# Optimization experiments

Measured on AMD Instinct MI355X. Metric: run time of the kernel, lower is better.

Reference implementation:

```python
import jax, jax.numpy as jnp
import numpy as np

B, C, H, W = 8, 384, 32, 32
KEYS, HEADS, U = 16, 4, 1
VS = C // HEADS
N = H * W
BN_EPS = 1e-5


def setup_inputs() -> dict:
    key = jax.random.key(0)
    ks = jax.random.split(key, 8)
    x = jax.random.normal(ks[0], (B, C, H, W), dtype=jnp.float32)
    # 1x1 convs (spectral-normalized in torch; SN only rescales the weight,
    # so a plain weight matrix computes the same functional form)
    Wq = jax.random.normal(ks[1], (KEYS * HEADS, C), dtype=jnp.float32) * 0.02
    Wk = jax.random.normal(ks[2], (KEYS * U, C), dtype=jnp.float32) * 0.02
    Wv = jax.random.normal(ks[3], (VS * U, C), dtype=jnp.float32) * 0.02
    # BatchNorm affine params (torch code xavier-inits weight, zeros bias)
    gamma_q = jax.random.normal(ks[4], (KEYS * HEADS,), dtype=jnp.float32)
    beta_q = jnp.zeros((KEYS * HEADS,), dtype=jnp.float32)
    gamma_v = jax.random.normal(ks[5], (VS * U,), dtype=jnp.float32)
    beta_v = jnp.zeros((VS * U,), dtype=jnp.float32)
    pos_emb = jax.random.normal(ks[6], (N, N, KEYS, U), dtype=jnp.float32)
    return {"x": x, "Wq": Wq, "Wk": Wk, "Wv": Wv,
            "gamma_q": gamma_q, "beta_q": beta_q,
            "gamma_v": gamma_v, "beta_v": beta_v,
            "pos_emb": pos_emb}


def _bn(z, gamma, beta):
    # z: (B, Ch, N); BatchNorm2d in training mode: biased batch stats over (B, N)
    mean = jnp.mean(z, axis=(0, 2), keepdims=True)
    var = jnp.var(z, axis=(0, 2), keepdims=True)
    zn = (z - mean) * jax.lax.rsqrt(var + BN_EPS)
    return zn * gamma[None, :, None] + beta[None, :, None]


def reference(x, Wq, Wk, Wv, gamma_q, beta_q, gamma_v, beta_v, pos_emb):
    xf = x.reshape(B, C, N)                       # 1x1 conv == per-pixel matmul
    q = jnp.einsum('oc,bcn->bon', Wq, xf)         # (B, KEYS*HEADS, N)
    k = jnp.einsum('oc,bcn->bon', Wk, xf)         # (B, KEYS*U, N)
    v = jnp.einsum('oc,bcn->bon', Wv, xf)         # (B, VS*U, N)
    q = _bn(q, gamma_q, beta_q)
    v = _bn(v, gamma_v, beta_v)
    q = q.reshape(B, HEADS, KEYS, N)
    k = k.reshape(B, U, KEYS, N)
    v = v.reshape(B, U, VS, N)
    k = jax.nn.softmax(k, axis=-1)
    lambdac = jnp.einsum('bukm,buvm->bkv', k, v)          # content lambda
    Yc = jnp.einsum('bhkn,bkv->bhvn', q, lambdac)
    lambdap = jnp.einsum('nmku,buvm->bnkv', pos_emb, v)   # position lambda (B,N,K,V)
    Yp = jnp.einsum('bhkn,bnkv->bhvn', q, lambdap)
    Y = (Yc + Yp).reshape(B, C, H, W)
    return Y
```

## Files before the change

### kernel.cpp

```cpp
#include <hip/hip_runtime.h>

typedef __attribute__((ext_vector_type(8))) short short8;
typedef __attribute__((ext_vector_type(16))) float floatx16;
typedef __attribute__((ext_vector_type(4))) float floatx4;
typedef unsigned short ushort16_t;
typedef unsigned int uint32;

#define BB 8
#define CC 384
#define NPIX 1024
#define TOTCH 176
#define BN_EPS 1e-5f

__device__ __forceinline__ ushort16_t f2bf(float x) {
    uint32 u = __float_as_uint(x);
    u += 0x7FFFu + ((u >> 16) & 1u);
    return (ushort16_t)(u >> 16);
}
__device__ __forceinline__ uint32 pk2(float a, float b) {
    uint32 ua = __float_as_uint(a); ua += 0x7FFFu + ((ua >> 16) & 1u);
    uint32 ub = __float_as_uint(b); ub += 0x7FFFu + ((ub >> 16) & 1u);
    return (ua >> 16) | (ub & 0xFFFF0000u);
}
__device__ __forceinline__ void dma16(const ushort16_t* g, ushort16_t* l) {
    __builtin_amdgcn_global_load_lds(
        (const __attribute__((address_space(1))) uint32*)g,
        (__attribute__((address_space(3))) uint32*)l, 16, 0, 0);
}


__global__ __launch_bounds__(256) void k_xt(const float* __restrict__ x,
    const float* __restrict__ Wq, const float* __restrict__ Wk,
    const float* __restrict__ Wv,
    ushort16_t* __restrict__ xbf, ushort16_t* __restrict__ wbf)
{
    int bx = blockIdx.x, t = threadIdx.x;
    if (bx < 384) {
        int gi = bx * 256 + t;
        int colg = gi & 2047;
        int cg   = gi >> 11;
        int b  = colg >> 8;
        int n0 = (colg & 255) * 4;
        int c0 = cg * 8;
        int col0 = colg * 4;
        float vv[8][4];
        #pragma unroll
        for (int j = 0; j < 8; ++j) {
            float4 f = *(const float4*)(x + (size_t)b * (CC * NPIX)
                                          + (size_t)(c0 + j) * NPIX + n0);
            vv[j][0] = f.x; vv[j][1] = f.y; vv[j][2] = f.z; vv[j][3] = f.w;
        }
        #pragma unroll
        for (int cc = 0; cc < 4; ++cc) {
            uint4 w;
            w.x = pk2(vv[0][cc], vv[1][cc]);
            w.y = pk2(vv[2][cc], vv[3][cc]);
            w.z = pk2(vv[4][cc], vv[5][cc]);
            w.w = pk2(vv[6][cc], vv[7][cc]);
            *(uint4*)&xbf[(size_t)(col0 + cc) * CC + c0] = w;
        }
    } else {
        int idx8 = (bx - 384) * 256 + t;
        int row = idx8 / 48;
        int j   = idx8 - row * 48;
        float4 f0, f1;
        if (row < 176) {
            const float* src;
            if (row < 64)       src = Wq + (size_t)row * CC;
            else if (row < 80)  src = Wk + (size_t)(row - 64) * CC;
            else                src = Wv + (size_t)(row - 80) * CC;
            f0 = *(const float4*)(src + j * 8);
            f1 = *(const float4*)(src + j * 8 + 4);
        } else {
            f0.x = f0.y = f0.z = f0.w = 0.f;
            f1 = f0;
        }
        uint4 w;
        w.x = pk2(f0.x, f0.y); w.y = pk2(f0.z, f0.w);
        w.z = pk2(f1.x, f1.y); w.w = pk2(f1.z, f1.w);
        *(uint4*)&wbf[(size_t)row * CC + j * 8] = w;
    }
}

__global__ __launch_bounds__(256) void k_proj(const ushort16_t* __restrict__ xbf,
    const ushort16_t* __restrict__ wbf, float* __restrict__ qkv)
{
    int t = threadIdx.x;
    int wave = t >> 6, lane = t & 63;
    int ct = blockIdx.x * 4 + wave;
    int r0 = blockIdx.y * 16;
    int col = ct * 16 + (lane & 15);
    int kh  = lane >> 4;
    const ushort16_t* ap = wbf + (size_t)(r0 + (lane & 15)) * CC + kh * 8;
    const ushort16_t* bp = xbf + (size_t)col * CC + kh * 8;
    floatx4 acc = {0.f, 0.f, 0.f, 0.f};
    short8 a0 = *(const short8*)ap;
    short8 b0 = *(const short8*)bp;
    #pragma unroll
    for (int k = 1; k < 12; ++k) {
        short8 a1 = *(const short8*)(ap + k * 32);
        short8 b1 = *(const short8*)(bp + k * 32);
        acc = __builtin_amdgcn_mfma_f32_16x16x32_bf16(a0, b0, acc, 0, 0, 0);
        a0 = a1; b0 = b1;
    }
    acc = __builtin_amdgcn_mfma_f32_16x16x32_bf16(a0, b0, acc, 0, 0, 0);
    int b = col >> 10, n = col & 1023;
    #pragma unroll
    for (int r = 0; r < 4; ++r) {
        int ch = r0 + (lane >> 4) * 4 + r;
        qkv[((size_t)b * TOTCH + ch) * NPIX + n] = acc[r];
    }
}

__global__ __launch_bounds__(256) void k_bnsm(const float* __restrict__ qkv,
    const float* __restrict__ gq, const float* __restrict__ bq,
    const float* __restrict__ gv, const float* __restrict__ bv,
    float* __restrict__ sA, float* __restrict__ sB, float* __restrict__ ksm)
{
    int bx = blockIdx.x, tid = threadIdx.x;
    int wid = tid >> 6, lane = tid & 63;
    if (bx < 160) {
        int ch = bx;
        int row; float gamma, beta;
        if (ch < 64) { row = ch; gamma = gq[ch]; beta = bq[ch]; }
        else { int j = ch - 64; row = 80 + j; gamma = gv[j]; beta = bv[j]; }
        float s = 0.f, ss = 0.f;
        for (int i = tid; i < BB * NPIX; i += 256) {
            int b = i >> 10, n = i & 1023;
            float val = qkv[((size_t)b * TOTCH + row) * NPIX + n];
            s += val; ss += val * val;
        }
        #pragma unroll
        for (int off = 32; off > 0; off >>= 1) {
            s  += __shfl_down(s, off);
            ss += __shfl_down(ss, off);
        }
        __shared__ float rs[4], rss[4];
        if (lane == 0) { rs[wid] = s; rss[wid] = ss; }
        __syncthreads();
        if (tid == 0) {
            float S  = rs[0] + rs[1] + rs[2] + rs[3];
            float SS = rss[0] + rss[1] + rss[2] + rss[3];
            float inv = 1.f / (BB * NPIX);
            float mean = S * inv;
            float var  = SS * inv - mean * mean;
            float a = gamma * rsqrtf(var + BN_EPS);
            sA[row] = a;
            sB[row] = beta - mean * a;
        }
    } else {
        int idx = bx - 160;
        int kc = idx & 15, b = idx >> 4;
        const float* rowp = qkv + ((size_t)b * TOTCH + 64 + kc) * NPIX;
        float v[4];
        #pragma unroll
        for (int j = 0; j < 4; ++j) v[j] = rowp[tid + 256 * j];
        float mx = fmaxf(fmaxf(v[0], v[1]), fmaxf(v[2], v[3]));
        #pragma unroll
        for (int off = 32; off > 0; off >>= 1) mx = fmaxf(mx, __shfl_down(mx, off));
        __shared__ float sm[4], ssum[4];
        if (lane == 0) sm[wid] = mx;
        __syncthreads();
        mx = fmaxf(fmaxf(sm[0], sm[1]), fmaxf(sm[2], sm[3]));
        float e[4], s = 0.f;
        #pragma unroll
        for (int j = 0; j < 4; ++j) { e[j] = __expf(v[j] - mx); s += e[j]; }
        #pragma unroll
        for (int off = 32; off > 0; off >>= 1) s += __shfl_down(s, off);
        if (lane == 0) ssum[wid] = s;
        __syncthreads();
        float inv = 1.f / (ssum[0] + ssum[1] + ssum[2] + ssum[3]);
        float* op = ksm + ((size_t)b * 16 + kc) * NPIX;
        #pragma unroll
        for (int j = 0; j < 4; ++j) op[tid + 256 * j] = e[j] * inv;
    }
}

__global__ __launch_bounds__(256) void k_pack(const float* __restrict__ qkv,
    const float* __restrict__ sA, const float* __restrict__ sB,
    ushort16_t* __restrict__ qt_g, ushort16_t* __restrict__ vt_g)
{
    int bx = blockIdx.x, t = threadIdx.x;
    if (bx < 128) {
        int bh = t & 31, nn = (t >> 5) & 7;
        int n = bx * 8 + nn;
        int b = bh >> 2, h = bh & 3;
        float vals[16];
        #pragma unroll
        for (int k = 0; k < 16; ++k) {
            int ch = h * 16 + k;
            vals[k] = qkv[((size_t)b * TOTCH + ch) * NPIX + n] * sA[ch] + sB[ch];
        }
        uint4 w0, w1;
        w0.x = pk2(vals[0], vals[1]);  w0.y = pk2(vals[2], vals[3]);
        w0.z = pk2(vals[4], vals[5]);  w0.w = pk2(vals[6], vals[7]);
        w1.x = pk2(vals[8], vals[9]);  w1.y = pk2(vals[10], vals[11]);
        w1.z = pk2(vals[12], vals[13]); w1.w = pk2(vals[14], vals[15]);
        *(uint4*)&qt_g[(size_t)n * 512 + bh * 8]       = w0;
        *(uint4*)&qt_g[(size_t)n * 512 + 256 + bh * 8] = w1;
    } else {
        int gi = (bx - 128) * 256 + t;
        int m8 = gi & 127;
        int vg = (gi >> 7) % 96;
        int b  = gi / (96 * 128);
        int m  = m8 * 8;
        int row = 80 + vg;
        float a = sA[row], bb = sB[row];
        const float* p = qkv + ((size_t)b * TOTCH + row) * NPIX + m;
        float4 f0 = *(const float4*)p;
        float4 f1 = *(const float4*)(p + 4);
        uint4 w;
        w.x = pk2(f0.x * a + bb, f0.y * a + bb);
        w.y = pk2(f0.z * a + bb, f0.w * a + bb);
        w.z = pk2(f1.x * a + bb, f1.y * a + bb);
        w.w = pk2(f1.z * a + bb, f1.w * a + bb);
        int mt = m >> 5, mq = (m >> 3) & 3;
        int vhh = vg / 48, vtt = (vg % 48) >> 4, vl = vg & 15;
        size_t idx = ((((size_t)b * 32 + mt) * 2 + vhh) * 3 + vtt) * 512
                   + mq * 128 + vl * 8;
        *(uint4*)&vt_g[idx] = w;
    }
}

__global__ __launch_bounds__(256) void k_lambdac(const float* __restrict__ ksm,
    const float* __restrict__ qkv, const float* __restrict__ sA,
    const float* __restrict__ sB, ushort16_t* __restrict__ lc_g)
{
    int v = blockIdx.x, b = blockIdx.y, tid = threadIdx.x;
    int row = 80 + v;
    float a = sA[row], bb = sB[row];
    const float* vp = qkv + ((size_t)b * TOTCH + row) * NPIX;
    const float* kp = ksm + (size_t)b * 16 * NPIX;
    float acc[16];
    #pragma unroll
    for (int k = 0; k < 16; ++k) acc[k] = 0.f;
    for (int m = tid; m < NPIX; m += 256) {
        float vv = vp[m] * a + bb;
        #pragma unroll
        for (int k = 0; k < 16; ++k) acc[k] += kp[k * NPIX + m] * vv;
    }
    #pragma unroll
    for (int k = 0; k < 16; ++k) {
        #pragma unroll
        for (int off = 32; off > 0; off >>= 1) acc[k] += __shfl_down(acc[k], off);
    }
    __shared__ float red[16][4];
    int wid = tid >> 6, lane = tid & 63;
    if (lane == 0) {
        #pragma unroll
        for (int k = 0; k < 16; ++k) red[k][wid] = acc[k];
    }
    __syncthreads();
    int vhh = v / 48, vtt = (v % 48) >> 4, vl = v & 15;
    size_t plane = ((size_t)(b * 2 + vhh) * 3 + vtt) * 512;
    if (tid < 16) {
        int k = tid;
        float val = red[k][0] + red[k][1] + red[k][2] + red[k][3];
        lc_g[plane + (k >> 3) * 128 + vl * 8 + (k & 7)] = f2bf(val);
    } else if (tid < 18) {
        int mq = 2 + (tid - 16);
        uint4 z; z.x = z.y = z.z = z.w = 0u;
        *(uint4*)&lc_g[plane + mq * 128 + vl * 8] = z;
    }
}

__global__ __launch_bounds__(512, 2) void k_main(const float* __restrict__ pos,
    const ushort16_t* __restrict__ qt_g, const ushort16_t* __restrict__ vt_g,
    const ushort16_t* __restrict__ lc_g, float* __restrict__ out)
{
    __shared__ __align__(16) ushort16_t q_s[4096];
    __shared__ __align__(16) ushort16_t P_s[4096];
    __shared__ __align__(16) ushort16_t V_s[12288];
    __shared__ __align__(16) ushort16_t S_s[8192];
    int tid  = threadIdx.x;
    int lane = tid & 63;
    int wave = tid >> 6;
    int n0 = blockIdx.x * 8;
    int vh = blockIdx.y;

    dma16(qt_g + (size_t)(n0 + wave) * 512 + lane * 8, &q_s[wave * 512]);

    floatx4 acc[2][3];
    #pragma unroll
    for (int hg = 0; hg < 2; ++hg)
        #pragma unroll
        for (int vt = 0; vt < 3; ++vt)
            acc[hg][vt] = floatx4{0.f, 0.f, 0.f, 0.f};

    int col1 = lane & 31, half = lane >> 5;
    int pb = col1 >> 2, ph = col1 & 3;
    int pplane = pb * 2 + (ph >> 1);
    int pf = pplane & 7;
    int pcb = ph & 1;
    int sm = tid & 31, snn = (tid >> 5) & 7, skh = (tid >> 8) & 1;
    int b2 = wave;

    for (int mt = 0; mt < 32; ++mt) {
        int m0 = mt * 32;
        __syncthreads();
        {
            const ushort16_t* src = vt_g
                + (size_t)(((b2 * 32 + mt) * 2 + vh) * 3) * 512;
            #pragma unroll
            for (int j = 0; j < 3; ++j)
                dma16(src + j * 512 + lane * 8, &V_s[b2 * 1536 + j * 512]);
        }
        {
            const float* p = pos + ((size_t)(n0 + snn) * 1024 + (m0 + sm)) * 16
                           + skh * 8;
            float4 f0 = *(const float4*)p;
            float4 f1 = *(const float4*)(p + 4);
            uint4 w;
            w.x = pk2(f0.x, f0.y); w.y = pk2(f0.z, f0.w);
            w.z = pk2(f1.x, f1.y); w.w = pk2(f1.z, f1.w);
            *(uint4*)&P_s[(snn * 2 + skh) * 256 + sm * 8] = w;
        }
        __syncthreads();
        {
            short8 afr = *(const short8*)&P_s[wave * 512 + half * 256 + col1 * 8];
            short8 bfr = *(const short8*)&q_s[wave * 512 + half * 256 + col1 * 8];
            floatx16 d;
            #pragma unroll
            for (int i = 0; i < 16; ++i) d[i] = 0.f;
            d = __builtin_amdgcn_mfma_f32_32x32x16_bf16(afr, bfr, d, 0, 0, 0);
            int nx = wave ^ pf;
            #pragma unroll
            for (int q = 0; q < 4; ++q) {
                int c = q * 16 + pcb * 8 + nx;
                uint2 wv;
                wv.x = pk2(d[q * 4 + 0], d[q * 4 + 1]);
                wv.y = pk2(d[q * 4 + 2], d[q * 4 + 3]);
                *(uint2*)&S_s[pplane * 512 + c * 8 + half * 4] = wv;
            }
        }
        __syncthreads();
        {
            short8 av[3];
            #pragma unroll
            for (int vt = 0; vt < 3; ++vt)
                av[vt] = *(const short8*)&V_s[b2 * 1536 + vt * 512 + lane * 8];
            #pragma unroll
            for (int hg = 0; hg < 2; ++hg) {
                int p2 = b2 * 2 + hg, f2 = p2 & 7;
                short8 bs = *(const short8*)&S_s[p2 * 512
                    + ((lane >> 4) * 16 + ((lane & 15) ^ f2)) * 8];
                #pragma unroll
                for (int vt = 0; vt < 3; ++vt)
                    acc[hg][vt] = __builtin_amdgcn_mfma_f32_16x16x32_bf16(
                        av[vt], bs, acc[hg][vt], 0, 0, 0);
            }
        }
    }

    __syncthreads();
    {
        const ushort16_t* src = lc_g + (size_t)((b2 * 2 + vh) * 3) * 512;
        #pragma unroll
        for (int j = 0; j < 3; ++j)
            dma16(src + j * 512 + lane * 8, &V_s[b2 * 1536 + j * 512]);
    }
    {
        int bh = tid & 31, nn = (tid >> 5) & 7, kh = (tid >> 8) & 1;
        int b_ = bh >> 2, h_ = bh & 3;
        int pl = b_ * 2 + (h_ >> 1), f = pl & 7;
        short8 qv = *(const short8*)&q_s[nn * 512 + kh * 256 + bh * 8];
        int c = kh * 16 + (h_ & 1) * 8 + (nn ^ f);
        *(short8*)&S_s[pl * 512 + c * 8] = qv;
        int zp = tid >> 5, zr = tid & 31;
        int zc = (2 + (zr >> 4)) * 16 + ((zr & 15) ^ (zp & 7));
        uint4 z; z.x = z.y = z.z = z.w = 0u;
        *(uint4*)&S_s[zp * 512 + zc * 8] = z;
    }
    __syncthreads();
    {
        short8 av[3];
        #pragma unroll
        for (int vt = 0; vt < 3; ++vt)
            av[vt] = *(const short8*)&V_s[b2 * 1536 + vt * 512 + lane * 8];
        #pragma unroll
        for (int hg = 0; hg < 2; ++hg) {
            int p2 = b2 * 2 + hg, f2 = p2 & 7;
            short8 bs = *(const short8*)&S_s[p2 * 512
                + ((lane >> 4) * 16 + ((lane & 15) ^ f2)) * 8];
            #pragma unroll
            for (int vt = 0; vt < 3; ++vt)
                acc[hg][vt] = __builtin_amdgcn_mfma_f32_16x16x32_bf16(
                    av[vt], bs, acc[hg][vt], 0, 0, 0);
        }
    }

    {
        int cn = lane & 15;
        int nloc = cn & 7;
        #pragma unroll
        for (int hg = 0; hg < 2; ++hg) {
            int h = hg * 2 + (cn >> 3);
            #pragma unroll
            for (int vt = 0; vt < 3; ++vt) {
                #pragma unroll
                for (int r = 0; r < 4; ++r) {
                    int v = vh * 48 + vt * 16 + (lane >> 4) * 4 + r;
                    out[(size_t)(b2 * 384 + h * 96 + v) * 1024 + n0 + nloc]
                        = acc[hg][vt][r];
                }
            }
        }
    }
}

extern "C" void kernel_launch(void* const* d_in, const int* in_sizes, int n_in,
                              void* d_out, int out_size, void* d_ws, size_t ws_size,
                              hipStream_t stream) {
    const float* x   = (const float*)d_in[0];
    const float* Wq  = (const float*)d_in[1];
    const float* Wk  = (const float*)d_in[2];
    const float* Wv  = (const float*)d_in[3];
    const float* gq  = (const float*)d_in[4];
    const float* bq  = (const float*)d_in[5];
    const float* gv  = (const float*)d_in[6];
    const float* bv  = (const float*)d_in[7];
    const float* pos = (const float*)d_in[8];
    float* out = (float*)d_out;
    float* ws  = (float*)d_ws;

    float* qkv = ws;
    float* sA  = ws + 1441792;
    float* sB  = ws + 1441968;
    float* ksm = ws + 1442144;
    ushort16_t* qt_g = (ushort16_t*)(ws + 1573216);
    ushort16_t* vt_g = (ushort16_t*)(ws + 1835360);
    ushort16_t* lc_g = (ushort16_t*)(ws + 2228576);
    ushort16_t* xbf  = (ushort16_t*)(ws + 2240864);
    ushort16_t* wbf  = (ushort16_t*)(ws + 3813728);

    k_xt<<<dim3(420), dim3(256), 0, stream>>>(x, Wq, Wk, Wv, xbf, wbf);
    k_proj<<<dim3(128, 11), dim3(256), 0, stream>>>(xbf, wbf, qkv);
    k_bnsm<<<dim3(288), dim3(256), 0, stream>>>(qkv, gq, bq, gv, bv, sA, sB, ksm);
    k_pack<<<dim3(512), dim3(256), 0, stream>>>(qkv, sA, sB, qt_g, vt_g);
    k_lambdac<<<dim3(96, 8), dim3(256), 0, stream>>>(ksm, qkv, sA, sB, lc_g);
    k_main<<<dim3(128, 2), dim3(512), 0, stream>>>(pos, qt_g, vt_g, lc_g, out);
}
```

Before: 203.9 us.

## Double-buffer pos/V tiles in main kernel, merge pack and lambdac, LDS-transpose x

The main kernel now double-buffers the pos_emb tile and the V tile. The next tile's global loads and DMA are issued while MFMA runs on the current one, which removes one barrier per iteration, and q is held in a register instead of LDS. k_pack and k_lambdac are merged into a single launch to save a kernel launch. The x-to-bf16 transpose now goes through an LDS tile so global writes are coalesced, the weight-conversion blocks each handle more work, and the BN/softmax loads use float4 vectors. The costs are more LDS in the main kernel, which may lower occupancy, and extra registers for the prefetched values.

New measurement: 184.8 us. -9.4%, faster.

```diff
diff --git a/kernel.cpp b/kernel.cpp
--- a/kernel.cpp
+++ b/kernel.cpp
@@ -26,6 +26,9 @@
     __builtin_amdgcn_global_load_lds(
         (const __attribute__((address_space(1))) uint32*)g,
         (__attribute__((address_space(3))) uint32*)l, 16, 0, 0);
+}
+__device__ __forceinline__ int div48(int x) {
+    return (int)(((unsigned)x * 21846u) >> 20);
 }
 
 
@@ -35,50 +38,54 @@
     ushort16_t* __restrict__ xbf, ushort16_t* __restrict__ wbf)
 {
     int bx = blockIdx.x, t = threadIdx.x;
-    if (bx < 384) {
-        int gi = bx * 256 + t;
-        int colg = gi & 2047;
-        int cg   = gi >> 11;
-        int b  = colg >> 8;
-        int n0 = (colg & 255) * 4;
-        int c0 = cg * 8;
-        int col0 = colg * 4;
-        float vv[8][4];
-        #pragma unroll
-        for (int j = 0; j < 8; ++j) {
-            float4 f = *(const float4*)(x + (size_t)b * (CC * NPIX)
-                                          + (size_t)(c0 + j) * NPIX + n0);
-            vv[j][0] = f.x; vv[j][1] = f.y; vv[j][2] = f.z; vv[j][3] = f.w;
-        }
-        #pragma unroll
-        for (int cc = 0; cc < 4; ++cc) {
+    if (bx < 256) {
+        __shared__ __align__(16) ushort16_t T[32 * 392];
+        int col0 = bx * 32;
+        int b = col0 >> 10, nbase = col0 & 1023;
+        const float* xb = x + (size_t)b * (CC * NPIX) + nbase;
+        #pragma unroll
+        for (int j = 0; j < 12; ++j) {
+            int idx = t + 256 * j;
+            int c = idx >> 3, ng = idx & 7;
+            float4 f = *(const float4*)(xb + (size_t)c * NPIX + ng * 4);
+            int n = ng * 4;
+            T[(n + 0) * 392 + c] = f2bf(f.x);
+            T[(n + 1) * 392 + c] = f2bf(f.y);
+            T[(n + 2) * 392 + c] = f2bf(f.z);
+            T[(n + 3) * 392 + c] = f2bf(f.w);
+        }
+        __syncthreads();
+        #pragma unroll
+        for (int j = 0; j < 6; ++j) {
+            int task = t + 256 * j;
+            int col = div48(task);
+            int ch  = task - col * 48;
+            uint4 w = *(const uint4*)&T[col * 392 + ch * 8];
+            *(uint4*)&xbf[(size_t)(col0 + col) * CC + ch * 8] = w;
+        }
+    } else {
+        #pragma unroll
+        for (int jj = 0; jj < 9; ++jj) {
+            int idx8 = ((bx - 256) * 9 + jj) * 256 + t;
+            int row = div48(idx8);
+            int g   = idx8 - row * 48;
+            float4 f0, f1;
+            if (row < 176) {
+                const float* src;
+                if (row < 64)       src = Wq + (size_t)row * CC;
+                else if (row < 80)  src = Wk + (size_t)(row - 64) * CC;
+                else                src = Wv + (size_t)(row - 80) * CC;
+                f0 = *(const float4*)(src + g * 8);
+                f1 = *(const float4*)(src + g * 8 + 4);
+            } else {
+                f0.x = f0.y = f0.z = f0.w = 0.f;
+                f1 = f0;
+            }
             uint4 w;
-            w.x = pk2(vv[0][cc], vv[1][cc]);
-            w.y = pk2(vv[2][cc], vv[3][cc]);
-            w.z = pk2(vv[4][cc], vv[5][cc]);
-            w.w = pk2(vv[6][cc], vv[7][cc]);
-            *(uint4*)&xbf[(size_t)(col0 + cc) * CC + c0] = w;
-        }
-    } else {
-        int idx8 = (bx - 384) * 256 + t;
-        int row = idx8 / 48;
-        int j   = idx8 - row * 48;
-        float4 f0, f1;
-        if (row < 176) {
-            const float* src;
-            if (row < 64)       src = Wq + (size_t)row * CC;
-            else if (row < 80)  src = Wk + (size_t)(row - 64) * CC;
-            else                src = Wv + (size_t)(row - 80) * CC;
-            f0 = *(const float4*)(src + j * 8);
-            f1 = *(const float4*)(src + j * 8 + 4);
-        } else {
-            f0.x = f0.y = f0.z = f0.w = 0.f;
-            f1 = f0;
-        }
-        uint4 w;
-        w.x = pk2(f0.x, f0.y); w.y = pk2(f0.z, f0.w);
-        w.z = pk2(f1.x, f1.y); w.w = pk2(f1.z, f1.w);
-        *(uint4*)&wbf[(size_t)row * CC + j * 8] = w;
+            w.x = pk2(f0.x, f0.y); w.y = pk2(f0.z, f0.w);
+            w.z = pk2(f1.x, f1.y); w.w = pk2(f1.z, f1.w);
+            *(uint4*)&wbf[(size_t)row * CC + g * 8] = w;
+        }
     }
 }
 
@@ -125,10 +132,14 @@
         if (ch < 64) { row = ch; gamma = gq[ch]; beta = bq[ch]; }
         else { int j = ch - 64; row = 80 + j; gamma = gv[j]; beta = bv[j]; }
         float s = 0.f, ss = 0.f;
-        for (int i = tid; i < BB * NPIX; i += 256) {
-            int b = i >> 10, n = i & 1023;
-            float val = qkv[((size_t)b * TOTCH + row) * NPIX + n];
-            s += val; ss += val * val;
+        #pragma unroll
+        for (int j = 0; j < 8; ++j) {
+            int i4 = tid + 256 * j;
+            int b = i4 >> 8, n4 = i4 & 255;
+            float4 f = *(const float4*)(qkv + ((size_t)b * TOTCH + row) * NPIX
+                                            + n4 * 4);
+            s  += f.x + f.y + f.z + f.w;
+            ss += f.x * f.x + f.y * f.y + f.z * f.z + f.w * f.w;
         }
         #pragma unroll
         for (int off = 32; off > 0; off >>= 1) {
@@ -152,9 +163,8 @@
         int idx = bx - 160;
         int kc = idx & 15, b = idx >> 4;
         const float* rowp = qkv + ((size_t)b * TOTCH + 64 + kc) * NPIX;
-        float v[4];
-        #pragma unroll
-        for (int j = 0; j < 4; ++j) v[j] = rowp[tid + 256 * j];
+        float4 v4 = *(const float4*)(rowp + tid * 4);
+        float v[4] = {v4.x, v4.y, v4.z, v4.w};
         float mx = fmaxf(fmaxf(v[0], v[1]), fmaxf(v[2], v[3]));
         #pragma unroll
         for (int off = 32; off > 0; off >>= 1) mx = fmaxf(mx, __shfl_down(mx, off));
@@ -170,15 +180,17 @@
         if (lane == 0) ssum[wid] = s;
         __syncthreads();
         float inv = 1.f / (ssum[0] + ssum[1] + ssum[2] + ssum[3]);
-        float* op = ksm + ((size_t)b * 16 + kc) * NPIX;
-        #pragma unroll
-        for (int j = 0; j < 4; ++j) op[tid + 256 * j] = e[j] * inv;
-    }
-}
-
-__global__ __launch_bounds__(256) void k_pack(const float* __restrict__ qkv,
+        float4 o;
+        o.x = e[0] * inv; o.y = e[1] * inv; o.z = e[2] * inv; o.w = e[3] * inv;
+        *(float4*)(ksm + ((size_t)b * 16 + kc) * NPIX + tid * 4) = o;
+    }
+}
+
+__global__ __launch_bounds__(256) void k_packlc(const float* __restrict__ qkv,
     const float* __restrict__ sA, const float* __restrict__ sB,
-    ushort16_t* __restrict__ qt_g, ushort16_t* __restrict__ vt_g)
+    const float* __restrict__ ksm,
+    ushort16_t* __restrict__ qt_g, ushort16_t* __restrict__ vt_g,
+    ushort16_t* __restrict__ lc_g)
 {
     int bx = blockIdx.x, t = threadIdx.x;
     if (bx < 128) {
@@ -198,7 +210,7 @@
         w1.z = pk2(vals[12], vals[13]); w1.w = pk2(vals[14], vals[15]);
         *(uint4*)&qt_g[(size_t)n * 512 + bh * 8]       = w0;
         *(uint4*)&qt_g[(size_t)n * 512 + 256 + bh * 8] = w1;
-    } else {
+    } else if (bx < 512) {
         int gi = (bx - 128) * 256 + t;
         int m8 = gi & 127;
         int vg = (gi >> 7) % 96;
@@ -219,48 +231,45 @@
         size_t idx = ((((size_t)b * 32 + mt) * 2 + vhh) * 3 + vtt) * 512
                    + mq * 128 + vl * 8;
         *(uint4*)&vt_g[idx] = w;
-    }
-}
-
-__global__ __launch_bounds__(256) void k_lambdac(const float* __restrict__ ksm,
-    const float* __restrict__ qkv, const float* __restrict__ sA,
-    const float* __restrict__ sB, ushort16_t* __restrict__ lc_g)
-{
-    int v = blockIdx.x, b = blockIdx.y, tid = threadIdx.x;
-    int row = 80 + v;
-    float a = sA[row], bb = sB[row];
-    const float* vp = qkv + ((size_t)b * TOTCH + row) * NPIX;
-    const float* kp = ksm + (size_t)b * 16 * NPIX;
-    float acc[16];
-    #pragma unroll
-    for (int k = 0; k < 16; ++k) acc[k] = 0.f;
-    for (int m = tid; m < NPIX; m += 256) {
-        float vv = vp[m] * a + bb;
-        #pragma unroll
-        for (int k = 0; k < 16; ++k) acc[k] += kp[k * NPIX + m] * vv;
-    }
-    #pragma unroll
-    for (int k = 0; k < 16; ++k) {
-        #pragma unroll
-        for (int off = 32; off > 0; off >>= 1) acc[k] += __shfl_down(acc[k], off);
-    }
-    __shared__ float red[16][4];
-    int wid = tid >> 6, lane = tid & 63;
-    if (lane == 0) {
-        #pragma unroll
-        for (int k = 0; k < 16; ++k) red[k][wid] = acc[k];
-    }
-    __syncthreads();
-    int vhh = v / 48, vtt = (v % 48) >> 4, vl = v & 15;
-    size_t plane = ((size_t)(b * 2 + vhh) * 3 + vtt) * 512;
-    if (tid < 16) {
-        int k = tid;
-        float val = red[k][0] + red[k][1] + red[k][2] + red[k][3];
-        lc_g[plane + (k >> 3) * 128 + vl * 8 + (k & 7)] = f2bf(val);
-    } else if (tid < 18) {
-        int mq = 2 + (tid - 16);
-        uint4 z; z.x = z.y = z.z = z.w = 0u;
-        *(uint4*)&lc_g[plane + mq * 128 + vl * 8] = z;
+    } else {
+        int gi = bx - 512;
+        int v = gi % 96, b = gi / 96;
+        int row = 80 + v;
+        float a = sA[row], bb = sB[row];
+        const float* vp = qkv + ((size_t)b * TOTCH + row) * NPIX;
+        const float* kp = ksm + (size_t)b * 16 * NPIX;
+        float acc[16];
+        #pragma unroll
+        for (int k = 0; k < 16; ++k) acc[k] = 0.f;
+        for (int m = t; m < NPIX; m += 256) {
+            float vv = vp[m] * a + bb;
+            #pragma unroll
+            for (int k = 0; k < 16; ++k) acc[k] += kp[k * NPIX + m] * vv;
+        }
+        #pragma unroll
+        for (int k = 0; k < 16; ++k) {
+            #pragma unroll
+            for (int off = 32; off > 0; off >>= 1)
+                acc[k] += __shfl_down(acc[k], off);
+        }
+        __shared__ float red[16][4];
+        int wid = t >> 6, lane = t & 63;
+        if (lane == 0) {
+            #pragma unroll
+            for (int k = 0; k < 16; ++k) red[k][wid] = acc[k];
+        }
+        __syncthreads();
+        int vhh = v / 48, vtt = (v % 48) >> 4, vl = v & 15;
+        size_t plane = ((size_t)(b * 2 + vhh) * 3 + vtt) * 512;
+        if (t < 16) {
+            int k = t;
+            float val = red[k][0] + red[k][1] + red[k][2] + red[k][3];
+            lc_g[plane + (k >> 3) * 128 + vl * 8 + (k & 7)] = f2bf(val);
+        } else if (t < 18) {
+            int mq = 2 + (t - 16);
+            uint4 z; z.x = z.y = z.z = z.w = 0u;
+            *(uint4*)&lc_g[plane + mq * 128 + vl * 8] = z;
+        }
     }
 }
 
@@ -268,24 +277,14 @@
     const ushort16_t* __restrict__ qt_g, const ushort16_t* __restrict__ vt_g,
     const ushort16_t* __restrict__ lc_g, float* __restrict__ out)
 {
-    __shared__ __align__(16) ushort16_t q_s[4096];
-    __shared__ __align__(16) ushort16_t P_s[4096];
-    __shared__ __align__(16) ushort16_t V_s[12288];
+    __shared__ __align__(16) ushort16_t P_s[8192];
+    __shared__ __align__(16) ushort16_t V_s[24576];
     __shared__ __align__(16) ushort16_t S_s[8192];
     int tid  = threadIdx.x;
     int lane = tid & 63;
     int wave = tid >> 6;
     int n0 = blockIdx.x * 8;
     int vh = blockIdx.y;
-
-    dma16(qt_g + (size_t)(n0 + wave) * 512 + lane * 8, &q_s[wave * 512]);
-
-    floatx4 acc[2][3];
-    #pragma unroll
-    for (int hg = 0; hg < 2; ++hg)
-        #pragma unroll
-        for (int vt = 0; vt < 3; ++vt)
-            acc[hg][vt] = floatx4{0.f, 0.f, 0.f, 0.f};
 
     int col1 = lane & 31, half = lane >> 5;
     int pb = col1 >> 2, ph = col1 & 3;
@@ -295,34 +294,46 @@
     int sm = tid & 31, snn = (tid >> 5) & 7, skh = (tid >> 8) & 1;
     int b2 = wave;
 
-    for (int mt = 0; mt < 32; ++mt) {
-        int m0 = mt * 32;
-        __syncthreads();
+    short8 qfr = *(const short8*)(qt_g + (size_t)(n0 + wave) * 512
+                                  + half * 256 + col1 * 8);
+
+    floatx4 acc[2][3];
+    #pragma unroll
+    for (int hg = 0; hg < 2; ++hg)
+        #pragma unroll
+        for (int vt = 0; vt < 3; ++vt)
+            acc[hg][vt] = floatx4{0.f, 0.f, 0.f, 0.f};
+
+    const float* pbase = pos + ((size_t)(n0 + snn) * 1024 + sm) * 16 + skh * 8;
+
+    {
+        float4 f0 = *(const float4*)pbase;
+        float4 f1 = *(const float4*)(pbase + 4);
+        uint4 w;
+        w.x = pk2(f0.x, f0.y); w.y = pk2(f0.z, f0.w);
+        w.z = pk2(f1.x, f1.y); w.w = pk2(f1.z, f1.w);
+        *(uint4*)&P_s[(snn * 2 + skh) * 256 + sm * 8] = w;
+        const ushort16_t* src = vt_g + (size_t)(((b2 * 32) * 2 + vh) * 3) * 512;
+        #pragma unroll
+        for (int j = 0; j < 3; ++j)
+            dma16(src + j * 512 + lane * 8, &V_s[b2 * 1536 + j * 512]);
+    }
+    __syncthreads();
+
+    for (int it = 0; it < 32; ++it) {
+        float4 pf0, pf1;
+        if (it < 31) {
+            const float* p = pbase + (size_t)(it + 1) * 32 * 16;
+            pf0 = *(const float4*)p;
+            pf1 = *(const float4*)(p + 4);
+        }
         {
-            const ushort16_t* src = vt_g
-                + (size_t)(((b2 * 32 + mt) * 2 + vh) * 3) * 512;
-            #pragma unroll
-            for (int j = 0; j < 3; ++j)
-                dma16(src + j * 512 + lane * 8, &V_s[b2 * 1536 + j * 512]);
-        }
-        {
-            const float* p = pos + ((size_t)(n0 + snn) * 1024 + (m0 + sm)) * 16
-                           + skh * 8;
-            float4 f0 = *(const float4*)p;
-            float4 f1 = *(const float4*)(p + 4);
-            uint4 w;
-            w.x = pk2(f0.x, f0.y); w.y = pk2(f0.z, f0.w);
-            w.z = pk2(f1.x, f1.y); w.w = pk2(f1.z, f1.w);
-            *(uint4*)&P_s[(snn * 2 + skh) * 256 + sm * 8] = w;
-        }
-        __syncthreads();
-        {
-            short8 afr = *(const short8*)&P_s[wave * 512 + half * 256 + col1 * 8];
-            short8 bfr = *(const short8*)&q_s[wave * 512 + half * 256 + col1 * 8];
+            short8 afr = *(const short8*)&P_s[(it & 1) * 4096
+                + wave * 512 + half * 256 + col1 * 8];
             floatx16 d;
             #pragma unroll
             for (int i = 0; i < 16; ++i) d[i] = 0.f;
-            d = __builtin_amdgcn_mfma_f32_32x32x16_bf16(afr, bfr, d, 0, 0, 0);
+            d = __builtin_amdgcn_mfma_f32_32x32x16_bf16(afr, qfr, d, 0, 0, 0);
             int nx = wave ^ pf;
             #pragma unroll
             for (int q = 0; q < 4; ++q) {
@@ -334,11 +345,20 @@
             }
         }
         __syncthreads();
+        if (it < 31) {
+            const ushort16_t* src = vt_g
+                + (size_t)(((b2 * 32 + it + 1) * 2 + vh) * 3) * 512;
+            #pragma unroll
+            for (int j = 0; j < 3; ++j)
+                dma16(src + j * 512 + lane * 8,
+                      &V_s[((it + 1) & 1) * 12288 + b2 * 1536 + j * 512]);
+        }
         {
+            int vb = (it & 1) * 12288;
             short8 av[3];
             #pragma unroll
             for (int vt = 0; vt < 3; ++vt)
-                av[vt] = *(const short8*)&V_s[b2 * 1536 + vt * 512 + lane * 8];
+                av[vt] = *(const short8*)&V_s[vb + b2 * 1536 + vt * 512 + lane * 8];
             #pragma unroll
             for (int hg = 0; hg < 2; ++hg) {
                 int p2 = b2 * 2 + hg, f2 = p2 & 7;
@@ -350,9 +370,15 @@
                         av[vt], bs, acc[hg][vt], 0, 0, 0);
             }
         }
-    }
-
-    __syncthreads();
+        if (it < 31) {
+            uint4 w;
+            w.x = pk2(pf0.x, pf0.y); w.y = pk2(pf0.z, pf0.w);
+            w.z = pk2(pf1.x, pf1.y); w.w = pk2(pf1.z, pf1.w);
+            *(uint4*)&P_s[((it + 1) & 1) * 4096 + (snn * 2 + skh) * 256 + sm * 8] = w;
+        }
+        __syncthreads();
+    }
+
     {
         const ushort16_t* src = lc_g + (size_t)((b2 * 2 + vh) * 3) * 512;
         #pragma unroll
@@ -360,12 +386,8 @@
             dma16(src + j * 512 + lane * 8, &V_s[b2 * 1536 + j * 512]);
     }
     {
-        int bh = tid & 31, nn = (tid >> 5) & 7, kh = (tid >> 8) & 1;
-        int b_ = bh >> 2, h_ = bh & 3;
-        int pl = b_ * 2 + (h_ >> 1), f = pl & 7;
-        short8 qv = *(const short8*)&q_s[nn * 512 + kh * 256 + bh * 8];
-        int c = kh * 16 + (h_ & 1) * 8 + (nn ^ f);
-        *(short8*)&S_s[pl * 512 + c * 8] = qv;
+        int c = half * 16 + pcb * 8 + (wave ^ pf);
+        *(short8*)&S_s[pplane * 512 + c * 8] = qfr;
         int zp = tid >> 5, zr = tid & 31;
         int zc = (2 + (zr >> 4)) * 16 + ((zr & 15) ^ (zp & 7));
         uint4 z; z.x = z.y = z.z = z.w = 0u;
@@ -433,10 +455,10 @@
     ushort16_t* xbf  = (ushort16_t*)(ws + 2240864);
     ushort16_t* wbf  = (ushort16_t*)(ws + 3813728);
 
-    k_xt<<<dim3(420), dim3(256), 0, stream>>>(x, Wq, Wk, Wv, xbf, wbf);
+    k_xt<<<dim3(260), dim3(256), 0, stream>>>(x, Wq, Wk, Wv, xbf, wbf);
     k_proj<<<dim3(128, 11), dim3(256), 0, stream>>>(xbf, wbf, qkv);
     k_bnsm<<<dim3(288), dim3(256), 0, stream>>>(qkv, gq, bq, gv, bv, sA, sB, ksm);
-    k_pack<<<dim3(512), dim3(256), 0, stream>>>(qkv, sA, sB, qt_g, vt_g);
-    k_lambdac<<<dim3(96, 8), dim3(256), 0, stream>>>(ksm, qkv, sA, sB, lc_g);
+    k_packlc<<<dim3(1280), dim3(256), 0, stream>>>(qkv, sA, sB, ksm,
+                                                   qt_g, vt_g, lc_g);
     k_main<<<dim3(128, 2), dim3(512), 0, stream>>>(pos, qt_g, vt_g, lc_g, out);
 }
```
